# Kernel optimization log

Measured on AMD Instinct MI355X. Metric: run time of the kernel, lower is better.

Reference implementation:

```python
import jax, jax.numpy as jnp
import numpy as np

CACHE_LEN = 1024
EPS = 1e-5

def layer_norm(x, g, b):
    m = jnp.mean(x, axis=-1, keepdims=True)
    var = jnp.mean(jnp.square(x - m), axis=-1, keepdims=True)
    return (x - m) * jax.lax.rsqrt(var + EPS) * g + b

def setup_inputs() -> dict:
    key = jax.random.key(0)
    ks = jax.random.split(key, 16)
    B, Lq, Lk, D_IN, D_OUT = 4, 4096, 5119, 512, 512
    s = 1.0 / np.sqrt(D_IN)
    return {
        "q": jax.random.normal(ks[0], (B, Lq, D_IN), jnp.float32),
        "k": jax.random.normal(ks[1], (B, Lk, D_IN), jnp.float32),
        "v": jax.random.normal(ks[2], (B, Lk, D_IN), jnp.float32),
        "gq": jnp.ones((D_IN,), jnp.float32),
        "bq": jnp.zeros((D_IN,), jnp.float32),
        "gk": jnp.ones((D_IN,), jnp.float32),
        "bk": jnp.zeros((D_IN,), jnp.float32),
        "gv": jnp.ones((D_IN,), jnp.float32),
        "bv": jnp.zeros((D_IN,), jnp.float32),
        "Wq": jax.random.uniform(ks[3], (D_IN, D_OUT), jnp.float32, -s, s),
        "bwq": jax.random.uniform(ks[4], (D_OUT,), jnp.float32, -s, s),
        "Wk": jax.random.uniform(ks[5], (D_IN, D_OUT), jnp.float32, -s, s),
        "bwk": jax.random.uniform(ks[6], (D_OUT,), jnp.float32, -s, s),
        "Wv": jax.random.uniform(ks[7], (D_IN, D_OUT), jnp.float32, -s, s),
        "bwv": jax.random.uniform(ks[8], (D_OUT,), jnp.float32, -s, s),
    }

def reference(q, k, v, gq, bq, gk, bk, gv, bv, Wq, bwq, Wk, bwk, Wv, bwv):
    B, Lq, _ = q.shape
    Lk = k.shape[1]
    qp = layer_norm(q, gq, bq) @ Wq + bwq            # [B,Lq,Do]
    kp = layer_norm(k, gk, bk) @ Wk + bwk            # [B,Lk,Do]
    vp = layer_norm(v, gv, bv) @ Wv + bwv            # [B,Lk,Do]
    kv = jax.nn.relu(kp) * vp                         # [B,Lk,Do]
    # integrate3 skew-pad builds a banded ones mask: query row i attends to
    # kv columns [sup+i, sup+i+cache_len-1]. Equivalent sliding-window sum
    # computed via prefix sums (O(Lk*d) instead of O(Lq*Lk*d)).
    sup = Lk - Lq - CACHE_LEN + 1
    cs = jnp.cumsum(kv, axis=1)
    cs = jnp.concatenate([jnp.zeros_like(cs[:, :1]), cs], axis=1)  # [B,Lk+1,Do]
    starts = sup + jnp.arange(Lq)
    weighted = cs[:, starts + CACHE_LEN] - cs[:, starts]            # [B,Lq,Do]
    return jax.nn.relu(qp) * weighted
```

## Files before the change

### kernel.cpp

```cpp
#include <hip/hip_runtime.h>

#define B     4
#define LQ    4096
#define LK    5119
#define D     512
#define CACHE 1024
#define MQ    (B * LQ)
#define MK    (B * LK)
#define MKP   20480
#define NCH   160
#define TI    32

typedef float  f32x4  __attribute__((ext_vector_type(4)));
typedef __bf16 bf16x2 __attribute__((ext_vector_type(2)));
typedef __bf16 bf16x4 __attribute__((ext_vector_type(4)));
typedef __bf16 bf16x8 __attribute__((ext_vector_type(8)));

__device__ __forceinline__ void async16(void* lds, const void* g)
{
    __builtin_amdgcn_global_load_lds(
        (__attribute__((address_space(1))) void*)(g),
        (__attribute__((address_space(3))) void*)(lds),
        16, 0, 0);
}

__global__ __launch_bounds__(64) void ln_kernel(
    const float* __restrict__ q, const float* __restrict__ k,
    const float* __restrict__ v,
    const float* __restrict__ gq, const float* __restrict__ bq,
    const float* __restrict__ gk, const float* __restrict__ bk,
    const float* __restrict__ gv, const float* __restrict__ bv,
    __bf16* __restrict__ qn, __bf16* __restrict__ kn, __bf16* __restrict__ vn)
{
    const int z = blockIdx.y;
    const float *x, *g, *bb; __bf16* o; int M;
    if (z == 0)      { x = q; g = gq; bb = bq; o = qn; M = MQ; }
    else if (z == 1) { x = k; g = gk; bb = bk; o = kn; M = MK; }
    else             { x = v; g = gv; bb = bv; o = vn; M = MK; }
    const int r = blockIdx.x;
    if (r >= M) return;

    const int t = threadIdx.x;
    const float* xr = x + (long)r * D;
    const float4 a0 = *reinterpret_cast<const float4*>(xr + t * 4);
    const float4 a1 = *reinterpret_cast<const float4*>(xr + 256 + t * 4);

    float s  = a0.x + a0.y + a0.z + a0.w + a1.x + a1.y + a1.z + a1.w;
    float ss = a0.x*a0.x + a0.y*a0.y + a0.z*a0.z + a0.w*a0.w
             + a1.x*a1.x + a1.y*a1.y + a1.z*a1.z + a1.w*a1.w;
#pragma unroll
    for (int m = 1; m < 64; m <<= 1) {
        s  += __shfl_xor(s,  m, 64);
        ss += __shfl_xor(ss, m, 64);
    }
    const float mean = s * (1.f / (float)D);
    const float var  = ss * (1.f / (float)D) - mean * mean;
    const float rs   = rsqrtf(var + 1e-5f);

    const float4 g0 = *reinterpret_cast<const float4*>(g + t * 4);
    const float4 g1 = *reinterpret_cast<const float4*>(g + 256 + t * 4);
    const float4 b0 = *reinterpret_cast<const float4*>(bb + t * 4);
    const float4 b1 = *reinterpret_cast<const float4*>(bb + 256 + t * 4);

    bf16x4 o0, o1;
    o0[0] = (__bf16)((a0.x - mean) * rs * g0.x + b0.x);
    o0[1] = (__bf16)((a0.y - mean) * rs * g0.y + b0.y);
    o0[2] = (__bf16)((a0.z - mean) * rs * g0.z + b0.z);
    o0[3] = (__bf16)((a0.w - mean) * rs * g0.w + b0.w);
    o1[0] = (__bf16)((a1.x - mean) * rs * g1.x + b1.x);
    o1[1] = (__bf16)((a1.y - mean) * rs * g1.y + b1.y);
    o1[2] = (__bf16)((a1.z - mean) * rs * g1.z + b1.z);
    o1[3] = (__bf16)((a1.w - mean) * rs * g1.w + b1.w);

    __bf16* orow = o + (long)r * D;
    *reinterpret_cast<bf16x4*>(orow + t * 4)       = o0;
    *reinterpret_cast<bf16x4*>(orow + 256 + t * 4) = o1;
}

__global__ __launch_bounds__(256) void wconv_kernel(
    const float* __restrict__ Wq, const float* __restrict__ Wk,
    const float* __restrict__ Wv,
    __bf16* __restrict__ wtq, __bf16* __restrict__ wtk, __bf16* __restrict__ wtv)
{
    const int z = blockIdx.z;
    const float* W = (z == 0) ? Wq : (z == 1) ? Wk : Wv;
    __bf16*     Wt = (z == 0) ? wtq : (z == 1) ? wtk : wtv;
    const int n  = blockIdx.x * 256 + threadIdx.x;
    const int k0 = blockIdx.y * 8;
    bf16x8 o;
#pragma unroll
    for (int j = 0; j < 8; ++j)
        o[j] = (__bf16)W[(long)(k0 + j) * D + n];
    *reinterpret_cast<bf16x8*>(Wt + (long)n * D + k0) = o;
}

__global__ __launch_bounds__(256) void gemm_q_kernel(
    const __bf16* __restrict__ A, const __bf16* __restrict__ Wt,
    const float* __restrict__ bias, __bf16* __restrict__ Cout)
{
    __shared__ __attribute__((aligned(16))) __bf16 As[128 * 32];
    __shared__ __attribute__((aligned(16))) __bf16 Bs[128 * 32];

    const int tid  = threadIdx.x;
    const int lane = tid & 63;
    const int wave = tid >> 6;
    const int quad = lane >> 4;
    const int l16  = lane & 15;
    const int wm   = wave >> 1;
    const int wn   = wave & 1;

    f32x4 acc[4][4];
#pragma unroll
    for (int i = 0; i < 4; ++i)
#pragma unroll
        for (int j = 0; j < 4; ++j)
            acc[i][j] = (f32x4){0.f, 0.f, 0.f, 0.f};

    const long arow0 = (long)blockIdx.x * 128;
    const long brow0 = (long)blockIdx.y * 128;
    const int  srow  = lane >> 2;
    const int  scol  = (lane & 3) * 8;

    for (int k0 = 0; k0 < D; k0 += 32) {
#pragma unroll
        for (int h = 0; h < 2; ++h) {
            const int chunk = h * 4 + wave;
            const int row   = chunk * 16 + srow;
            async16(&As[chunk * 512], &A [(arow0 + row) * D + k0 + scol]);
            async16(&Bs[chunk * 512], &Wt[(brow0 + row) * D + k0 + scol]);
        }
        __syncthreads();

        bf16x8 af[4], bfr[4];
#pragma unroll
        for (int tm = 0; tm < 4; ++tm)
            af[tm] = *reinterpret_cast<const bf16x8*>(
                &As[(wm * 64 + tm * 16 + l16) * 32 + quad * 8]);
#pragma unroll
        for (int tn = 0; tn < 4; ++tn)
            bfr[tn] = *reinterpret_cast<const bf16x8*>(
                &Bs[(wn * 64 + tn * 16 + l16) * 32 + quad * 8]);

#pragma unroll
        for (int tm = 0; tm < 4; ++tm)
#pragma unroll
            for (int tn = 0; tn < 4; ++tn)
                acc[tm][tn] = __builtin_amdgcn_mfma_f32_16x16x32_bf16(
                    af[tm], bfr[tn], acc[tm][tn], 0, 0, 0);
        __syncthreads();
    }

#pragma unroll
    for (int tm = 0; tm < 4; ++tm) {
        const long row0 = arow0 + wm * 64 + tm * 16 + quad * 4;
#pragma unroll
        for (int tn = 0; tn < 4; ++tn) {
            const int col = (int)brow0 + wn * 64 + tn * 16 + l16;
            const float bv = bias[col];
#pragma unroll
            for (int r = 0; r < 4; ++r)
                Cout[(row0 + r) * D + col] =
                    (__bf16)fmaxf(acc[tm][tn][r] + bv, 0.f);
        }
    }
}

__global__ __launch_bounds__(256) void gemm_kv_kernel(
    const __bf16* __restrict__ Ak, const __bf16* __restrict__ Av,
    const __bf16* __restrict__ Wtk, const __bf16* __restrict__ Wtv,
    const float* __restrict__ bk, const float* __restrict__ bv,
    __bf16* __restrict__ kvout)
{
    __shared__ __attribute__((aligned(16))) __bf16 Ks [128 * 32];
    __shared__ __attribute__((aligned(16))) __bf16 Vs [128 * 32];
    __shared__ __attribute__((aligned(16))) __bf16 WKs[128 * 32];
    __shared__ __attribute__((aligned(16))) __bf16 WVs[128 * 32];

    const int tid  = threadIdx.x;
    const int lane = tid & 63;
    const int wave = tid >> 6;
    const int quad = lane >> 4;
    const int l16  = lane & 15;
    const int wm   = wave >> 1;
    const int wn   = wave & 1;

    f32x4 acck[4][4], accv[4][4];
#pragma unroll
    for (int i = 0; i < 4; ++i)
#pragma unroll
        for (int j = 0; j < 4; ++j) {
            acck[i][j] = (f32x4){0.f, 0.f, 0.f, 0.f};
            accv[i][j] = (f32x4){0.f, 0.f, 0.f, 0.f};
        }

    const long arow0 = (long)blockIdx.x * 128;
    const long brow0 = (long)blockIdx.y * 128;
    const int  srow  = lane >> 2;
    const int  scol  = (lane & 3) * 8;

    for (int k0 = 0; k0 < D; k0 += 32) {
#pragma unroll
        for (int h = 0; h < 2; ++h) {
            const int chunk = h * 4 + wave;
            const int row   = chunk * 16 + srow;
            async16(&Ks [chunk * 512], &Ak [(arow0 + row) * D + k0 + scol]);
            async16(&Vs [chunk * 512], &Av [(arow0 + row) * D + k0 + scol]);
            async16(&WKs[chunk * 512], &Wtk[(brow0 + row) * D + k0 + scol]);
            async16(&WVs[chunk * 512], &Wtv[(brow0 + row) * D + k0 + scol]);
        }
        __syncthreads();

        bf16x8 fa[4], fb[4];
#pragma unroll
        for (int tm = 0; tm < 4; ++tm)
            fa[tm] = *reinterpret_cast<const bf16x8*>(
                &Ks[(wm * 64 + tm * 16 + l16) * 32 + quad * 8]);
#pragma unroll
        for (int tn = 0; tn < 4; ++tn)
            fb[tn] = *reinterpret_cast<const bf16x8*>(
                &WKs[(wn * 64 + tn * 16 + l16) * 32 + quad * 8]);
#pragma unroll
        for (int tm = 0; tm < 4; ++tm)
#pragma unroll
            for (int tn = 0; tn < 4; ++tn)
                acck[tm][tn] = __builtin_amdgcn_mfma_f32_16x16x32_bf16(
                    fa[tm], fb[tn], acck[tm][tn], 0, 0, 0);

#pragma unroll
        for (int tm = 0; tm < 4; ++tm)
            fa[tm] = *reinterpret_cast<const bf16x8*>(
                &Vs[(wm * 64 + tm * 16 + l16) * 32 + quad * 8]);
#pragma unroll
        for (int tn = 0; tn < 4; ++tn)
            fb[tn] = *reinterpret_cast<const bf16x8*>(
                &WVs[(wn * 64 + tn * 16 + l16) * 32 + quad * 8]);
#pragma unroll
        for (int tm = 0; tm < 4; ++tm)
#pragma unroll
            for (int tn = 0; tn < 4; ++tn)
                accv[tm][tn] = __builtin_amdgcn_mfma_f32_16x16x32_bf16(
                    fa[tm], fb[tn], accv[tm][tn], 0, 0, 0);
        __syncthreads();
    }

#pragma unroll
    for (int tm = 0; tm < 4; ++tm) {
        const long row0 = arow0 + wm * 64 + tm * 16 + quad * 4;
#pragma unroll
        for (int tn = 0; tn < 4; ++tn) {
            const int col = (int)brow0 + wn * 64 + tn * 16 + l16;
            const float bkc = bk[col];
            const float bvc = bv[col];
#pragma unroll
            for (int r = 0; r < 4; ++r) {
                const float kp = fmaxf(acck[tm][tn][r] + bkc, 0.f);
                const float vp = accv[tm][tn][r] + bvc;
                kvout[(row0 + r) * D + col] = (__bf16)(kp * vp);
            }
        }
    }
}

__global__ __launch_bounds__(256) void chunk_kernel(
    const __bf16* __restrict__ kv, float* __restrict__ Csum)
{
    const int c    = blockIdx.x;
    const int b    = blockIdx.y;
    const int col2 = threadIdx.x * 2;
    const __bf16* base = kv + ((long)b * LK + (long)c * 32) * D + col2;
    float s0 = 0.f, s1 = 0.f;
#pragma unroll
    for (int j = 0; j < 32; ++j) {
        const bf16x2 vv = *reinterpret_cast<const bf16x2*>(base + (long)j * D);
        s0 += (float)vv[0];
        s1 += (float)vv[1];
    }
    float* o = Csum + ((long)b * NCH + c) * D + col2;
    o[0] = s0; o[1] = s1;
}

__global__ __launch_bounds__(256) void window_kernel(
    const __bf16* __restrict__ kv, const float* __restrict__ Csum,
    const __bf16* __restrict__ qpb, float* __restrict__ out)
{
    const int iq   = blockIdx.x;
    const int b    = blockIdx.y;
    const int i0   = iq * TI;
    const int col2 = threadIdx.x * 2;

    const float* cs = Csum + (long)b * NCH * D + col2;
    float s0 = 0.f, s1 = 0.f;
#pragma unroll
    for (int c = 0; c < 32; ++c) {
        const float2 cv = *reinterpret_cast<const float2*>(cs + (long)(iq + c) * D);
        s0 += cv.x; s1 += cv.y;
    }

    const __bf16* kvb = kv  + (long)b * LK * D + col2;
    const __bf16* qb  = qpb + (long)b * LQ * D + col2;
    float*        ob  = out + (long)b * LQ * D + col2;

#pragma unroll 8
    for (int i = i0; i < i0 + TI; ++i) {
        const bf16x2 qv = *reinterpret_cast<const bf16x2*>(qb + (long)i * D);
        *reinterpret_cast<float2*>(ob + (long)i * D) =
            make_float2((float)qv[0] * s0, (float)qv[1] * s1);
        const bf16x2 lead  = *reinterpret_cast<const bf16x2*>(kvb + (long)(i + CACHE) * D);
        const bf16x2 trail = *reinterpret_cast<const bf16x2*>(kvb + (long)i * D);
        s0 += (float)lead[0] - (float)trail[0];
        s1 += (float)lead[1] - (float)trail[1];
    }
}

extern "C" void kernel_launch(void* const* d_in, const int* in_sizes, int n_in,
                              void* d_out, int out_size, void* d_ws, size_t ws_size,
                              hipStream_t stream)
{
    const float* q   = (const float*)d_in[0];
    const float* k   = (const float*)d_in[1];
    const float* v   = (const float*)d_in[2];
    const float* gq  = (const float*)d_in[3];
    const float* bq  = (const float*)d_in[4];
    const float* gk  = (const float*)d_in[5];
    const float* bk  = (const float*)d_in[6];
    const float* gv  = (const float*)d_in[7];
    const float* bv  = (const float*)d_in[8];
    const float* Wq  = (const float*)d_in[9];
    const float* bwq = (const float*)d_in[10];
    const float* Wk  = (const float*)d_in[11];
    const float* bwk = (const float*)d_in[12];
    const float* Wv  = (const float*)d_in[13];
    const float* bwv = (const float*)d_in[14];
    float* out = (float*)d_out;

    char* ws = (char*)d_ws;
    __bf16* qn   = (__bf16*)ws;
    __bf16* kn   = qn  + (long)MQ  * D;
    __bf16* vn   = kn  + (long)MKP * D;
    __bf16* qpb  = vn  + (long)MKP * D;
    __bf16* kvb  = qpb + (long)MQ  * D;
    __bf16* wtq  = kvb + (long)MKP * D;
    __bf16* wtk  = wtq + (long)D * D;
    __bf16* wtv  = wtk + (long)D * D;
    float*  Csum = (float*)(wtv + (long)D * D);

    ln_kernel<<<dim3(MK, 3), 64, 0, stream>>>(q, k, v, gq, bq, gk, bk, gv, bv,
                                              qn, kn, vn);
    wconv_kernel<<<dim3(2, 64, 3), 256, 0, stream>>>(Wq, Wk, Wv, wtq, wtk, wtv);

    gemm_q_kernel<<<dim3(MQ / 128, D / 128), 256, 0, stream>>>(qn, wtq, bwq, qpb);

    gemm_kv_kernel<<<dim3(MKP / 128, D / 128), 256, 0, stream>>>(
        kn, vn, wtk, wtv, bwk, bwv, kvb);

    chunk_kernel<<<dim3(NCH, B), 256, 0, stream>>>(kvb, Csum);

    window_kernel<<<dim3(LQ / TI, B), 256, 0, stream>>>(kvb, Csum, qpb, out);
}
```

Baseline: 273.0 us.

## Widen GEMM K-tile with XOR-swizzled LDS, shrink kv N-tile, batch LN rows

The layer-norm kernel now processes 8 rows per 256-thread block, with 32 lanes per row and 16 contiguous columns per lane, replacing one 64-thread block per row. Both GEMMs move from 32-wide to 64-wide K tiles in LDS, using an XOR swizzle on 16-byte chunks to avoid bank conflicts, and get launch_bounds occupancy hints. The fused K/V GEMM halves its N tile to 64, which reduces accumulator registers and doubles the grid. The larger LDS footprint and halved loop trip count trade against more K/V activation reloads from the narrower N tile.

New measurement: 237.9 us. 1.15x faster.

```diff
diff --git a/kernel.cpp b/kernel.cpp
--- a/kernel.cpp
+++ b/kernel.cpp
@@ -24,7 +24,7 @@
         16, 0, 0);
 }
 
-__global__ __launch_bounds__(64) void ln_kernel(
+__global__ __launch_bounds__(256) void ln_kernel(
     const float* __restrict__ q, const float* __restrict__ k,
     const float* __restrict__ v,
     const float* __restrict__ gq, const float* __restrict__ bq,
@@ -37,19 +37,25 @@
     if (z == 0)      { x = q; g = gq; bb = bq; o = qn; M = MQ; }
     else if (z == 1) { x = k; g = gk; bb = bk; o = kn; M = MK; }
     else             { x = v; g = gv; bb = bv; o = vn; M = MK; }
-    const int r = blockIdx.x;
+    const int r = blockIdx.x * 8 + (threadIdx.x >> 5);
     if (r >= M) return;
 
-    const int t = threadIdx.x;
-    const float* xr = x + (long)r * D;
-    const float4 a0 = *reinterpret_cast<const float4*>(xr + t * 4);
-    const float4 a1 = *reinterpret_cast<const float4*>(xr + 256 + t * 4);
-
-    float s  = a0.x + a0.y + a0.z + a0.w + a1.x + a1.y + a1.z + a1.w;
-    float ss = a0.x*a0.x + a0.y*a0.y + a0.z*a0.z + a0.w*a0.w
-             + a1.x*a1.x + a1.y*a1.y + a1.z*a1.z + a1.w*a1.w;
-#pragma unroll
-    for (int m = 1; m < 64; m <<= 1) {
+    const int c0 = (threadIdx.x & 31) * 16;
+    const float* xr = x + (long)r * D + c0;
+
+    float4 a[4];
+#pragma unroll
+    for (int j = 0; j < 4; ++j)
+        a[j] = *reinterpret_cast<const float4*>(xr + j * 4);
+
+    float s = 0.f, ss = 0.f;
+#pragma unroll
+    for (int j = 0; j < 4; ++j) {
+        s  += a[j].x + a[j].y + a[j].z + a[j].w;
+        ss += a[j].x*a[j].x + a[j].y*a[j].y + a[j].z*a[j].z + a[j].w*a[j].w;
+    }
+#pragma unroll
+    for (int m = 1; m <= 16; m <<= 1) {
         s  += __shfl_xor(s,  m, 64);
         ss += __shfl_xor(ss, m, 64);
     }
@@ -57,24 +63,26 @@
     const float var  = ss * (1.f / (float)D) - mean * mean;
     const float rs   = rsqrtf(var + 1e-5f);
 
-    const float4 g0 = *reinterpret_cast<const float4*>(g + t * 4);
-    const float4 g1 = *reinterpret_cast<const float4*>(g + 256 + t * 4);
-    const float4 b0 = *reinterpret_cast<const float4*>(bb + t * 4);
-    const float4 b1 = *reinterpret_cast<const float4*>(bb + 256 + t * 4);
-
-    bf16x4 o0, o1;
-    o0[0] = (__bf16)((a0.x - mean) * rs * g0.x + b0.x);
-    o0[1] = (__bf16)((a0.y - mean) * rs * g0.y + b0.y);
-    o0[2] = (__bf16)((a0.z - mean) * rs * g0.z + b0.z);
-    o0[3] = (__bf16)((a0.w - mean) * rs * g0.w + b0.w);
-    o1[0] = (__bf16)((a1.x - mean) * rs * g1.x + b1.x);
-    o1[1] = (__bf16)((a1.y - mean) * rs * g1.y + b1.y);
-    o1[2] = (__bf16)((a1.z - mean) * rs * g1.z + b1.z);
-    o1[3] = (__bf16)((a1.w - mean) * rs * g1.w + b1.w);
-
-    __bf16* orow = o + (long)r * D;
-    *reinterpret_cast<bf16x4*>(orow + t * 4)       = o0;
-    *reinterpret_cast<bf16x4*>(orow + 256 + t * 4) = o1;
+    bf16x8 o0, o1;
+#pragma unroll
+    for (int j = 0; j < 4; ++j) {
+        const float4 gv4 = *reinterpret_cast<const float4*>(g  + c0 + j * 4);
+        const float4 bv4 = *reinterpret_cast<const float4*>(bb + c0 + j * 4);
+        const float y0 = (a[j].x - mean) * rs * gv4.x + bv4.x;
+        const float y1 = (a[j].y - mean) * rs * gv4.y + bv4.y;
+        const float y2 = (a[j].z - mean) * rs * gv4.z + bv4.z;
+        const float y3 = (a[j].w - mean) * rs * gv4.w + bv4.w;
+        if (j < 2) {
+            o0[j*4+0] = (__bf16)y0; o0[j*4+1] = (__bf16)y1;
+            o0[j*4+2] = (__bf16)y2; o0[j*4+3] = (__bf16)y3;
+        } else {
+            o1[(j-2)*4+0] = (__bf16)y0; o1[(j-2)*4+1] = (__bf16)y1;
+            o1[(j-2)*4+2] = (__bf16)y2; o1[(j-2)*4+3] = (__bf16)y3;
+        }
+    }
+    __bf16* orow = o + (long)r * D + c0;
+    *reinterpret_cast<bf16x8*>(orow)     = o0;
+    *reinterpret_cast<bf16x8*>(orow + 8) = o1;
 }
 
 __global__ __launch_bounds__(256) void wconv_kernel(
@@ -94,12 +102,12 @@
     *reinterpret_cast<bf16x8*>(Wt + (long)n * D + k0) = o;
 }
 
-__global__ __launch_bounds__(256) void gemm_q_kernel(
+__global__ __launch_bounds__(256, 2) void gemm_q_kernel(
     const __bf16* __restrict__ A, const __bf16* __restrict__ Wt,
     const float* __restrict__ bias, __bf16* __restrict__ Cout)
 {
-    __shared__ __attribute__((aligned(16))) __bf16 As[128 * 32];
-    __shared__ __attribute__((aligned(16))) __bf16 Bs[128 * 32];
+    __shared__ __attribute__((aligned(16))) __bf16 As[128 * 64];
+    __shared__ __attribute__((aligned(16))) __bf16 Bs[128 * 64];
 
     const int tid  = threadIdx.x;
     const int lane = tid & 63;
@@ -118,35 +126,45 @@
 
     const long arow0 = (long)blockIdx.x * 128;
     const long brow0 = (long)blockIdx.y * 128;
-    const int  srow  = lane >> 2;
-    const int  scol  = (lane & 3) * 8;
-
-    for (int k0 = 0; k0 < D; k0 += 32) {
-#pragma unroll
-        for (int h = 0; h < 2; ++h) {
-            const int chunk = h * 4 + wave;
-            const int row   = chunk * 16 + srow;
-            async16(&As[chunk * 512], &A [(arow0 + row) * D + k0 + scol]);
-            async16(&Bs[chunk * 512], &Wt[(brow0 + row) * D + k0 + scol]);
+    const int  lrow  = lane >> 3;
+    const int  lcs   = ((lane & 7) ^ lrow) * 8;
+
+    for (int k0 = 0; k0 < D; k0 += 64) {
+#pragma unroll
+        for (int j = 0; j < 4; ++j) {
+            const int r0  = (j * 4 + wave) * 8;
+            const int row = r0 + lrow;
+            async16(&As[r0 * 64], &A [(arow0 + row) * D + k0 + lcs]);
+            async16(&Bs[r0 * 64], &Wt[(brow0 + row) * D + k0 + lcs]);
         }
         __syncthreads();
 
-        bf16x8 af[4], bfr[4];
-#pragma unroll
-        for (int tm = 0; tm < 4; ++tm)
-            af[tm] = *reinterpret_cast<const bf16x8*>(
-                &As[(wm * 64 + tm * 16 + l16) * 32 + quad * 8]);
-#pragma unroll
-        for (int tn = 0; tn < 4; ++tn)
-            bfr[tn] = *reinterpret_cast<const bf16x8*>(
-                &Bs[(wn * 64 + tn * 16 + l16) * 32 + quad * 8]);
-
-#pragma unroll
-        for (int tm = 0; tm < 4; ++tm)
-#pragma unroll
-            for (int tn = 0; tn < 4; ++tn)
-                acc[tm][tn] = __builtin_amdgcn_mfma_f32_16x16x32_bf16(
-                    af[tm], bfr[tn], acc[tm][tn], 0, 0, 0);
+        bf16x8 af[4][2], bf[4][2];
+#pragma unroll
+        for (int tm = 0; tm < 4; ++tm) {
+            const int m = wm * 64 + tm * 16 + l16;
+#pragma unroll
+            for (int kh = 0; kh < 2; ++kh)
+                af[tm][kh] = *reinterpret_cast<const bf16x8*>(
+                    &As[m * 64 + (((kh * 4 + quad) ^ (m & 7)) * 8)]);
+        }
+#pragma unroll
+        for (int tn = 0; tn < 4; ++tn) {
+            const int n = wn * 64 + tn * 16 + l16;
+#pragma unroll
+            for (int kh = 0; kh < 2; ++kh)
+                bf[tn][kh] = *reinterpret_cast<const bf16x8*>(
+                    &Bs[n * 64 + (((kh * 4 + quad) ^ (n & 7)) * 8)]);
+        }
+
+#pragma unroll
+        for (int kh = 0; kh < 2; ++kh)
+#pragma unroll
+            for (int tm = 0; tm < 4; ++tm)
+#pragma unroll
+                for (int tn = 0; tn < 4; ++tn)
+                    acc[tm][tn] = __builtin_amdgcn_mfma_f32_16x16x32_bf16(
+                        af[tm][kh], bf[tn][kh], acc[tm][tn], 0, 0, 0);
         __syncthreads();
     }
 
@@ -165,16 +183,16 @@
     }
 }
 
-__global__ __launch_bounds__(256) void gemm_kv_kernel(
+__global__ __launch_bounds__(256, 2) void gemm_kv_kernel(
     const __bf16* __restrict__ Ak, const __bf16* __restrict__ Av,
     const __bf16* __restrict__ Wtk, const __bf16* __restrict__ Wtv,
     const float* __restrict__ bk, const float* __restrict__ bv,
     __bf16* __restrict__ kvout)
 {
-    __shared__ __attribute__((aligned(16))) __bf16 Ks [128 * 32];
-    __shared__ __attribute__((aligned(16))) __bf16 Vs [128 * 32];
-    __shared__ __attribute__((aligned(16))) __bf16 WKs[128 * 32];
-    __shared__ __attribute__((aligned(16))) __bf16 WVs[128 * 32];
+    __shared__ __attribute__((aligned(16))) __bf16 Ks [128 * 64];
+    __shared__ __attribute__((aligned(16))) __bf16 Vs [128 * 64];
+    __shared__ __attribute__((aligned(16))) __bf16 WKs[64 * 64];
+    __shared__ __attribute__((aligned(16))) __bf16 WVs[64 * 64];
 
     const int tid  = threadIdx.x;
     const int lane = tid & 63;
@@ -184,62 +202,86 @@
     const int wm   = wave >> 1;
     const int wn   = wave & 1;
 
-    f32x4 acck[4][4], accv[4][4];
+    f32x4 acck[4][2], accv[4][2];
 #pragma unroll
     for (int i = 0; i < 4; ++i)
 #pragma unroll
-        for (int j = 0; j < 4; ++j) {
+        for (int j = 0; j < 2; ++j) {
             acck[i][j] = (f32x4){0.f, 0.f, 0.f, 0.f};
             accv[i][j] = (f32x4){0.f, 0.f, 0.f, 0.f};
         }
 
     const long arow0 = (long)blockIdx.x * 128;
-    const long brow0 = (long)blockIdx.y * 128;
-    const int  srow  = lane >> 2;
-    const int  scol  = (lane & 3) * 8;
-
-    for (int k0 = 0; k0 < D; k0 += 32) {
-#pragma unroll
-        for (int h = 0; h < 2; ++h) {
-            const int chunk = h * 4 + wave;
-            const int row   = chunk * 16 + srow;
-            async16(&Ks [chunk * 512], &Ak [(arow0 + row) * D + k0 + scol]);
-            async16(&Vs [chunk * 512], &Av [(arow0 + row) * D + k0 + scol]);
-            async16(&WKs[chunk * 512], &Wtk[(brow0 + row) * D + k0 + scol]);
-            async16(&WVs[chunk * 512], &Wtv[(brow0 + row) * D + k0 + scol]);
+    const long brow0 = (long)blockIdx.y * 64;
+    const int  lrow  = lane >> 3;
+    const int  lcs   = ((lane & 7) ^ lrow) * 8;
+
+    for (int k0 = 0; k0 < D; k0 += 64) {
+#pragma unroll
+        for (int j = 0; j < 4; ++j) {
+            const int r0  = (j * 4 + wave) * 8;
+            const int row = r0 + lrow;
+            async16(&Ks[r0 * 64], &Ak[(arow0 + row) * D + k0 + lcs]);
+            async16(&Vs[r0 * 64], &Av[(arow0 + row) * D + k0 + lcs]);
+        }
+#pragma unroll
+        for (int j = 0; j < 2; ++j) {
+            const int r0  = (j * 4 + wave) * 8;
+            const int row = r0 + lrow;
+            async16(&WKs[r0 * 64], &Wtk[(brow0 + row) * D + k0 + lcs]);
+            async16(&WVs[r0 * 64], &Wtv[(brow0 + row) * D + k0 + lcs]);
         }
         __syncthreads();
 
-        bf16x8 fa[4], fb[4];
-#pragma unroll
-        for (int tm = 0; tm < 4; ++tm)
-            fa[tm] = *reinterpret_cast<const bf16x8*>(
-                &Ks[(wm * 64 + tm * 16 + l16) * 32 + quad * 8]);
-#pragma unroll
-        for (int tn = 0; tn < 4; ++tn)
-            fb[tn] = *reinterpret_cast<const bf16x8*>(
-                &WKs[(wn * 64 + tn * 16 + l16) * 32 + quad * 8]);
-#pragma unroll
-        for (int tm = 0; tm < 4; ++tm)
-#pragma unroll
-            for (int tn = 0; tn < 4; ++tn)
-                acck[tm][tn] = __builtin_amdgcn_mfma_f32_16x16x32_bf16(
-                    fa[tm], fb[tn], acck[tm][tn], 0, 0, 0);
-
-#pragma unroll
-        for (int tm = 0; tm < 4; ++tm)
-            fa[tm] = *reinterpret_cast<const bf16x8*>(
-                &Vs[(wm * 64 + tm * 16 + l16) * 32 + quad * 8]);
-#pragma unroll
-        for (int tn = 0; tn < 4; ++tn)
-            fb[tn] = *reinterpret_cast<const bf16x8*>(
-                &WVs[(wn * 64 + tn * 16 + l16) * 32 + quad * 8]);
-#pragma unroll
-        for (int tm = 0; tm < 4; ++tm)
-#pragma unroll
-            for (int tn = 0; tn < 4; ++tn)
-                accv[tm][tn] = __builtin_amdgcn_mfma_f32_16x16x32_bf16(
-                    fa[tm], fb[tn], accv[tm][tn], 0, 0, 0);
+        bf16x8 fa[4][2], fb[2][2];
+#pragma unroll
+        for (int tm = 0; tm < 4; ++tm) {
+            const int m = wm * 64 + tm * 16 + l16;
+#pragma unroll
+            for (int kh = 0; kh < 2; ++kh)
+                fa[tm][kh] = *reinterpret_cast<const bf16x8*>(
+                    &Ks[m * 64 + (((kh * 4 + quad) ^ (m & 7)) * 8)]);
+        }
+#pragma unroll
+        for (int tn = 0; tn < 2; ++tn) {
+            const int n = wn * 32 + tn * 16 + l16;
+#pragma unroll
+            for (int kh = 0; kh < 2; ++kh)
+                fb[tn][kh] = *reinterpret_cast<const bf16x8*>(
+                    &WKs[n * 64 + (((kh * 4 + quad) ^ (n & 7)) * 8)]);
+        }
+#pragma unroll
+        for (int kh = 0; kh < 2; ++kh)
+#pragma unroll
+            for (int tm = 0; tm < 4; ++tm)
+#pragma unroll
+                for (int tn = 0; tn < 2; ++tn)
+                    acck[tm][tn] = __builtin_amdgcn_mfma_f32_16x16x32_bf16(
+                        fa[tm][kh], fb[tn][kh], acck[tm][tn], 0, 0, 0);
+#pragma unroll
+        for (int tm = 0; tm < 4; ++tm) {
+            const int m = wm * 64 + tm * 16 + l16;
+#pragma unroll
+            for (int kh = 0; kh < 2; ++kh)
+                fa[tm][kh] = *reinterpret_cast<const bf16x8*>(
+                    &Vs[m * 64 + (((kh * 4 + quad) ^ (m & 7)) * 8)]);
+        }
+#pragma unroll
+        for (int tn = 0; tn < 2; ++tn) {
+            const int n = wn * 32 + tn * 16 + l16;
+#pragma unroll
+            for (int kh = 0; kh < 2; ++kh)
+                fb[tn][kh] = *reinterpret_cast<const bf16x8*>(
+                    &WVs[n * 64 + (((kh * 4 + quad) ^ (n & 7)) * 8)]);
+        }
+#pragma unroll
+        for (int kh = 0; kh < 2; ++kh)
+#pragma unroll
+            for (int tm = 0; tm < 4; ++tm)
+#pragma unroll
+                for (int tn = 0; tn < 2; ++tn)
+                    accv[tm][tn] = __builtin_amdgcn_mfma_f32_16x16x32_bf16(
+                        fa[tm][kh], fb[tn][kh], accv[tm][tn], 0, 0, 0);
         __syncthreads();
     }
 
@@ -247,8 +289,8 @@
     for (int tm = 0; tm < 4; ++tm) {
         const long row0 = arow0 + wm * 64 + tm * 16 + quad * 4;
 #pragma unroll
-        for (int tn = 0; tn < 4; ++tn) {
-            const int col = (int)brow0 + wn * 64 + tn * 16 + l16;
+        for (int tn = 0; tn < 2; ++tn) {
+            const int col = (int)brow0 + wn * 32 + tn * 16 + l16;
             const float bkc = bk[col];
             const float bvc = bv[col];
 #pragma unroll
@@ -344,13 +386,13 @@
     __bf16* wtv  = wtk + (long)D * D;
     float*  Csum = (float*)(wtv + (long)D * D);
 
-    ln_kernel<<<dim3(MK, 3), 64, 0, stream>>>(q, k, v, gq, bq, gk, bk, gv, bv,
-                                              qn, kn, vn);
+    ln_kernel<<<dim3(2560, 3), 256, 0, stream>>>(q, k, v, gq, bq, gk, bk, gv, bv,
+                                                 qn, kn, vn);
     wconv_kernel<<<dim3(2, 64, 3), 256, 0, stream>>>(Wq, Wk, Wv, wtq, wtk, wtv);
 
     gemm_q_kernel<<<dim3(MQ / 128, D / 128), 256, 0, stream>>>(qn, wtq, bwq, qpb);
 
-    gemm_kv_kernel<<<dim3(MKP / 128, D / 128), 256, 0, stream>>>(
+    gemm_kv_kernel<<<dim3(MKP / 128, D / 64), 256, 0, stream>>>(
         kn, vn, wtk, wtv, bwk, bwv, kvb);
 
     chunk_kernel<<<dim3(NCH, B), 256, 0, stream>>>(kvb, Csum);
```
